# Kernel tuning notes

Hardware: AMD Instinct MI355X
Metric: run time of the kernel (lower is better)

Reference implementation:

```python
import jax, jax.numpy as jnp
import numpy as np

IM_SIZE = (256, 256)
OVERSAMP = 1.25
WIDTH = 6
BETA = float(np.pi * np.sqrt((WIDTH / OVERSAMP * (OVERSAMP - 0.5)) ** 2 - 0.8))
OS_SIZE = tuple(int(np.ceil(OVERSAMP * n)) for n in IM_SIZE)  # (320, 320)
D = 2


def _kb(x):
    # Kaiser-Bessel interpolation kernel: i0(beta*sqrt(1-x^2)) for |x|<=1 (sigpy convention)
    return jnp.i0(BETA * jnp.sqrt(jnp.maximum(1.0 - x * x, 0.0)))


def setup_inputs() -> dict:
    key = jax.random.key(0)
    k1, k2, k3 = jax.random.split(key, 3)
    N, C = 1, 8
    img_r = jax.random.normal(k1, (N, C) + IM_SIZE, dtype=jnp.float32)
    img_i = jax.random.normal(k2, (N, C) + IM_SIZE, dtype=jnp.float32)
    # trajectory in [-N_i/2, N_i/2] per the class docstring
    trj = (jax.random.uniform(k3, (N, 64, 4096, D), dtype=jnp.float32) - 0.5) * 256.0
    return {"img_r": img_r, "img_i": img_i, "trj": trj}


def _nufft_forward(img_r, img_i, trj):
    img = (img_r + 1j * img_i).astype(jnp.complex64)  # (N, C, H, W)
    nd = img.ndim
    # --- apodization (inverse FT of KB kernel), separable per axis ---
    for a in range(D):
        n, osn = IM_SIZE[a], OS_SIZE[a]
        idx = jnp.arange(n, dtype=jnp.float32)
        arg = jnp.sqrt(BETA ** 2 - (np.pi * WIDTH * (idx - n // 2) / osn) ** 2)
        apod = arg / jnp.sinh(arg)
        shape = [1] * nd
        shape[nd - D + a] = n
        img = img * apod.reshape(shape)
    # --- scale + centered zero-pad to oversampled grid ---
    img = img / np.sqrt(float(np.prod(IM_SIZE)))
    pads = [(0, 0)] * (nd - D) + [(((o - n) // 2), (o - n) - ((o - n) // 2))
                                  for n, o in zip(IM_SIZE, OS_SIZE)]
    img = jnp.pad(img, pads)
    # --- centered FFT (ifftshift -> fftn(norm=None) -> fftshift) ---
    axes = tuple(range(-D, 0))
    ksp_os = jnp.fft.fftshift(jnp.fft.fftn(jnp.fft.ifftshift(img, axes=axes), axes=axes), axes=axes)
    # --- scale trajectory to oversampled grid coordinates ---
    scale = jnp.array([OS_SIZE[a] / IM_SIZE[a] for a in range(D)], jnp.float32)
    shift = jnp.array([OS_SIZE[a] // 2 for a in range(D)], jnp.float32)
    coord = trj * scale + shift  # (N, R, S, 2)
    x0 = jnp.ceil(coord - WIDTH / 2.0)
    # --- KB interpolation: fixed 6x6 neighbor loop, vectorized gather over all points ---
    N = img.shape[0]
    out = jnp.zeros((N,) + img.shape[1:nd - D] + coord.shape[1:-1], jnp.complex64)

    def gather(grid, ix, iy):  # grid (C, Hos, Wos), ix/iy (R, S) -> (C, R, S)
        return grid[:, ix, iy]

    for dx in range(WIDTH):
        px = x0[..., 0] + dx
        wx = _kb((px - coord[..., 0]) / (WIDTH / 2.0))
        ix = px.astype(jnp.int32) % OS_SIZE[0]
        for dy in range(WIDTH):
            py = x0[..., 1] + dy
            wy = _kb((py - coord[..., 1]) / (WIDTH / 2.0))
            iy = py.astype(jnp.int32) % OS_SIZE[1]
            vals = jax.vmap(gather)(ksp_os, ix, iy)  # (N, C, R, S)
            out = out + vals * (wx * wy)[:, None, :, :]
    return out / (WIDTH ** D)


def reference(img_r, img_i, trj):
    return _nufft_forward(img_r, img_i, trj)
```

## Files before the change

kernel.cpp:

```cpp
#include <hip/hip_runtime.h>
#include <math.h>

#define NCH   8
#define IMN   256
#define OSN   320
#define NPTS  (64*4096)
#define KD    512
#define BETA_F   10.9551078f
#define BETA2_F  120.014389f
#define APOD_C   0.05890486225f
#define GROWS 326
#define GCOLS 328
#define GPITCH (GCOLS * NCH)

typedef unsigned short u16;
typedef unsigned int   u32;
typedef __attribute__((ext_vector_type(8))) short s16x8;
typedef __attribute__((ext_vector_type(4))) float f32x4;
typedef __attribute__((ext_vector_type(2))) float f32x2;

__device__ __forceinline__ u32 f2bf(float f) {
    u32 u = __float_as_uint(f);
    return (u + 0x7FFFu + ((u >> 16) & 1u)) >> 16;
}

__device__ __forceinline__ float i0f(float t) {
    if (t < 3.75f) {
        float y = t * t * (1.0f / 14.0625f);
        return 1.0f + y * (3.5156229f + y * (3.0899424f + y * (1.2067492f +
                     y * (0.2659732f + y * (0.0360768f + y * 0.0045813f)))));
    }
    float z = 3.75f / t;
    float p = 0.39894228f + z * (0.01328592f + z * (0.00225319f + z * (-0.00157565f +
              z * (0.00916281f + z * (-0.02057706f + z * (0.02635537f +
              z * (-0.01647633f + z * 0.00392377f)))))));
    return expf(t) * rsqrtf(t) * p;
}

__device__ __forceinline__ float apodf(int i) {
    float x = APOD_C * (float)(i - IMN / 2);
    float arg = sqrtf(BETA2_F - x * x);
    float e = expf(arg);
    float sh = 0.5f * (e - 1.0f / e);
    return arg / sh;
}

__global__ void prep(const float* __restrict__ r, const float* __restrict__ im,
                     u32* __restrict__ B1, u32* __restrict__ B2,
                     u32* __restrict__ A) {
    const int b = blockIdx.x, t = threadIdx.x;
    if (b < (OSN * IMN) / 256) {
        int idx = b * 256 + t;
        int k = idx >> 8, j = idx & 255;
        int p = (k * (j + 32)) % OSN;
        float th = (2.0f * (float)M_PI / (float)OSN) * (float)p;
        float s = ((k + j) & 1) ? -1.0f : 1.0f;
        float sn, cs;
        sincosf(th, &sn, &cs);
        float re = s * cs, imv = -s * sn;
        B1[idx] = f2bf(re) | (f2bf(-imv) << 16);
        B2[idx] = f2bf(imv) | (f2bf(re) << 16);
    } else {
        int idx = (b - (OSN * IMN) / 256) * 256 + t;
        int i2 = idx & 255, i1 = (idx >> 8) & 255;
        float w = apodf(i1) * apodf(i2) * (1.0f / 256.0f);
        A[idx] = f2bf(r[idx] * w) | (f2bf(im[idx] * w) << 16);
    }
}

__launch_bounds__(64)
__global__ void gemm1(const short* __restrict__ Abf, const short* __restrict__ B1,
                      const short* __restrict__ B2, short* __restrict__ Tb) {
    const int c = blockIdx.z;
    const int mBase = blockIdx.y * 32;
    const int nBase = blockIdx.x * 32;
    __shared__ short As[2][32][36], B1s[2][32][36], B2s[2][32][36];
    const int t = threadIdx.x;
    const int row = t >> 1, seg = (t & 1) * 16;
    const int fm = t & 15, fq = (t >> 4) * 8;
    const short* ap  = Abf + (long)(c * IMN + mBase + row) * KD + seg;
    const short* b1p = B1 + (long)(nBase + row) * KD + seg;
    const short* b2p = B2 + (long)(nBase + row) * KD + seg;
    f32x4 zz = {0.f, 0.f, 0.f, 0.f};
    f32x4 accRe[2][2], accIm[2][2];
    #pragma unroll
    for (int i = 0; i < 2; i++)
        #pragma unroll
        for (int j = 0; j < 2; j++) { accRe[i][j] = zz; accIm[i][j] = zz; }

    s16x8 c0 = *(const s16x8*)(ap);
    s16x8 c1 = *(const s16x8*)(ap + 8);
    s16x8 c2 = *(const s16x8*)(b1p);
    s16x8 c3 = *(const s16x8*)(b1p + 8);
    s16x8 c4 = *(const s16x8*)(b2p);
    s16x8 c5 = *(const s16x8*)(b2p + 8);

    #pragma unroll
    for (int kc = 0; kc < 16; kc++) {
        const int buf = kc & 1;
        *(s16x8*)&As [buf][row][seg]     = c0;
        *(s16x8*)&As [buf][row][seg + 8] = c1;
        *(s16x8*)&B1s[buf][row][seg]     = c2;
        *(s16x8*)&B1s[buf][row][seg + 8] = c3;
        *(s16x8*)&B2s[buf][row][seg]     = c4;
        *(s16x8*)&B2s[buf][row][seg + 8] = c5;
        if (kc < 15) {
            const int kb = (kc + 1) * 32;
            c0 = *(const s16x8*)(ap + kb);
            c1 = *(const s16x8*)(ap + kb + 8);
            c2 = *(const s16x8*)(b1p + kb);
            c3 = *(const s16x8*)(b1p + kb + 8);
            c4 = *(const s16x8*)(b2p + kb);
            c5 = *(const s16x8*)(b2p + kb + 8);
        }
        s16x8 a0  = *(const s16x8*)&As [buf][fm][fq];
        s16x8 a1  = *(const s16x8*)&As [buf][16 + fm][fq];
        s16x8 b10 = *(const s16x8*)&B1s[buf][fm][fq];
        s16x8 b11 = *(const s16x8*)&B1s[buf][16 + fm][fq];
        s16x8 b20 = *(const s16x8*)&B2s[buf][fm][fq];
        s16x8 b21 = *(const s16x8*)&B2s[buf][16 + fm][fq];
        accRe[0][0] = __builtin_amdgcn_mfma_f32_16x16x32_bf16(a0, b10, accRe[0][0], 0, 0, 0);
        accRe[0][1] = __builtin_amdgcn_mfma_f32_16x16x32_bf16(a0, b11, accRe[0][1], 0, 0, 0);
        accRe[1][0] = __builtin_amdgcn_mfma_f32_16x16x32_bf16(a1, b10, accRe[1][0], 0, 0, 0);
        accRe[1][1] = __builtin_amdgcn_mfma_f32_16x16x32_bf16(a1, b11, accRe[1][1], 0, 0, 0);
        accIm[0][0] = __builtin_amdgcn_mfma_f32_16x16x32_bf16(a0, b20, accIm[0][0], 0, 0, 0);
        accIm[0][1] = __builtin_amdgcn_mfma_f32_16x16x32_bf16(a0, b21, accIm[0][1], 0, 0, 0);
        accIm[1][0] = __builtin_amdgcn_mfma_f32_16x16x32_bf16(a1, b20, accIm[1][0], 0, 0, 0);
        accIm[1][1] = __builtin_amdgcn_mfma_f32_16x16x32_bf16(a1, b21, accIm[1][1], 0, 0, 0);
    }
    #pragma unroll
    for (int i = 0; i < 2; i++)
        #pragma unroll
        for (int j = 0; j < 2; j++) {
            int i1b = mBase + i * 16 + (t >> 4) * 4;
            int k2  = nBase + j * 16 + fm;
            s16x8 v;
            #pragma unroll
            for (int r = 0; r < 4; r++) {
                v[2 * r]     = (short)f2bf(accRe[i][j][r]);
                v[2 * r + 1] = (short)f2bf(accIm[i][j][r]);
            }
            *(s16x8*)(Tb + ((long)(c * OSN + k2)) * KD + 2 * i1b) = v;
        }
}

__launch_bounds__(64)
__global__ void gemm2(const short* __restrict__ B1, const short* __restrict__ B2,
                      const short* __restrict__ Tb, u32* __restrict__ Gb) {
    const int c = blockIdx.z;
    const int mBase = blockIdx.y * 32;
    const int nBase = blockIdx.x * 32;
    __shared__ short A1s[2][32][36], A2s[2][32][36], Bs[2][32][36];
    const int t = threadIdx.x;
    const int row = t >> 1, seg = (t & 1) * 16;
    const int fm = t & 15, fq = (t >> 4) * 8;
    const short* a1p = B1 + (long)(mBase + row) * KD + seg;
    const short* a2p = B2 + (long)(mBase + row) * KD + seg;
    const short* bp  = Tb + ((long)(c * OSN + nBase + row)) * KD + seg;
    f32x4 zz = {0.f, 0.f, 0.f, 0.f};
    f32x4 accRe[2][2], accIm[2][2];
    #pragma unroll
    for (int i = 0; i < 2; i++)
        #pragma unroll
        for (int j = 0; j < 2; j++) { accRe[i][j] = zz; accIm[i][j] = zz; }

    s16x8 c0 = *(const s16x8*)(a1p);
    s16x8 c1 = *(const s16x8*)(a1p + 8);
    s16x8 c2 = *(const s16x8*)(a2p);
    s16x8 c3 = *(const s16x8*)(a2p + 8);
    s16x8 c4 = *(const s16x8*)(bp);
    s16x8 c5 = *(const s16x8*)(bp + 8);

    #pragma unroll
    for (int kc = 0; kc < 16; kc++) {
        const int buf = kc & 1;
        *(s16x8*)&A1s[buf][row][seg]     = c0;
        *(s16x8*)&A1s[buf][row][seg + 8] = c1;
        *(s16x8*)&A2s[buf][row][seg]     = c2;
        *(s16x8*)&A2s[buf][row][seg + 8] = c3;
        *(s16x8*)&Bs [buf][row][seg]     = c4;
        *(s16x8*)&Bs [buf][row][seg + 8] = c5;
        if (kc < 15) {
            const int kb = (kc + 1) * 32;
            c0 = *(const s16x8*)(a1p + kb);
            c1 = *(const s16x8*)(a1p + kb + 8);
            c2 = *(const s16x8*)(a2p + kb);
            c3 = *(const s16x8*)(a2p + kb + 8);
            c4 = *(const s16x8*)(bp + kb);
            c5 = *(const s16x8*)(bp + kb + 8);
        }
        s16x8 a10 = *(const s16x8*)&A1s[buf][fm][fq];
        s16x8 a11 = *(const s16x8*)&A1s[buf][16 + fm][fq];
        s16x8 a20 = *(const s16x8*)&A2s[buf][fm][fq];
        s16x8 a21 = *(const s16x8*)&A2s[buf][16 + fm][fq];
        s16x8 b0  = *(const s16x8*)&Bs [buf][fm][fq];
        s16x8 b1  = *(const s16x8*)&Bs [buf][16 + fm][fq];
        accRe[0][0] = __builtin_amdgcn_mfma_f32_16x16x32_bf16(a10, b0, accRe[0][0], 0, 0, 0);
        accRe[0][1] = __builtin_amdgcn_mfma_f32_16x16x32_bf16(a10, b1, accRe[0][1], 0, 0, 0);
        accRe[1][0] = __builtin_amdgcn_mfma_f32_16x16x32_bf16(a11, b0, accRe[1][0], 0, 0, 0);
        accRe[1][1] = __builtin_amdgcn_mfma_f32_16x16x32_bf16(a11, b1, accRe[1][1], 0, 0, 0);
        accIm[0][0] = __builtin_amdgcn_mfma_f32_16x16x32_bf16(a20, b0, accIm[0][0], 0, 0, 0);
        accIm[0][1] = __builtin_amdgcn_mfma_f32_16x16x32_bf16(a20, b1, accIm[0][1], 0, 0, 0);
        accIm[1][0] = __builtin_amdgcn_mfma_f32_16x16x32_bf16(a21, b0, accIm[1][0], 0, 0, 0);
        accIm[1][1] = __builtin_amdgcn_mfma_f32_16x16x32_bf16(a21, b1, accIm[1][1], 0, 0, 0);
    }
    #pragma unroll
    for (int i = 0; i < 2; i++)
        #pragma unroll
        for (int j = 0; j < 2; j++) {
            int k2 = nBase + j * 16 + fm;
            int pc  = k2 + 3;
            int pc2 = (k2 < 3) ? (k2 + 323) : ((k2 >= 317) ? (k2 - 317) : -1);
            #pragma unroll
            for (int r = 0; r < 4; r++) {
                int k1 = mBase + i * 16 + (t >> 4) * 4 + r;
                u32 val = f2bf(accRe[i][j][r]) | (f2bf(accIm[i][j][r]) << 16);
                int pr  = k1 + 3;
                int pr2 = (k1 < 3) ? (k1 + 323) : ((k1 >= 317) ? (k1 - 317) : -1);
                Gb[(long)pr * GPITCH + pc * NCH + c] = val;
                if (pr2 >= 0)              Gb[(long)pr2 * GPITCH + pc  * NCH + c] = val;
                if (pc2 >= 0)              Gb[(long)pr  * GPITCH + pc2 * NCH + c] = val;
                if (pr2 >= 0 && pc2 >= 0)  Gb[(long)pr2 * GPITCH + pc2 * NCH + c] = val;
            }
        }
}

__global__ void interp_kernel(const float* __restrict__ trj,
                              const u32* __restrict__ grid,
                              u32* __restrict__ out) {
    const int t = threadIdx.x;
    __shared__ float wxs[128][6], wys[128][6];
    __shared__ int   x0s[128], y0s[128];

    {
        int ptl = t & 127, axis = t >> 7;
        int pt = blockIdx.x * 128 + ptl;
        float tv = trj[pt * 2 + axis];
        float cc = __fadd_rn(__fmul_rn(tv, 1.25f), 160.0f);
        float v0 = ceilf(__fadd_rn(cc, -3.0f));
        if (axis) y0s[ptl] = (int)v0; else x0s[ptl] = (int)v0;
        float* ws = axis ? wys[ptl] : wxs[ptl];
        #pragma unroll
        for (int d = 0; d < 6; d++) {
            float u = __fdiv_rn(__fsub_rn(v0 + (float)d, cc), 3.0f);
            ws[d] = i0f(BETA_F * sqrtf(fmaxf(1.0f - u * u, 0.0f)));
        }
    }
    __syncthreads();

    const int pl = t >> 1;
    const int h = t & 1;
    float wx[6], wy[6];
    #pragma unroll
    for (int d = 0; d < 6; d++) { wx[d] = wxs[pl][d]; wy[d] = wys[pl][d]; }
    const int px = x0s[pl] + 3;
    const int py = y0s[pl] + 3;
    const u32* g0 = grid + (long)px * GPITCH + py * NCH + h * 4;

    uint4 buf[2][6];
    #pragma unroll
    for (int dy = 0; dy < 6; dy++) buf[0][dy] = *(const uint4*)(g0 + dy * NCH);

    f32x2 a0 = {0.f, 0.f}, a1 = {0.f, 0.f}, a2 = {0.f, 0.f}, a3 = {0.f, 0.f};
    #pragma unroll
    for (int dx = 0; dx < 6; dx++) {
        if (dx < 5) {
            const u32* gn = g0 + (dx + 1) * GPITCH;
            #pragma unroll
            for (int dy = 0; dy < 6; dy++)
                buf[(dx + 1) & 1][dy] = *(const uint4*)(gn + dy * NCH);
        }
        float wxv = wx[dx];
        #pragma unroll
        for (int dy = 0; dy < 6; dy++) {
            uint4 g = buf[dx & 1][dy];
            float ww = wxv * wy[dy];
            f32x2 w2 = {ww, ww};
            f32x2 v0v = { __uint_as_float(g.x << 16), __uint_as_float(g.x & 0xFFFF0000u) };
            f32x2 v1v = { __uint_as_float(g.y << 16), __uint_as_float(g.y & 0xFFFF0000u) };
            f32x2 v2v = { __uint_as_float(g.z << 16), __uint_as_float(g.z & 0xFFFF0000u) };
            f32x2 v3v = { __uint_as_float(g.w << 16), __uint_as_float(g.w & 0xFFFF0000u) };
            a0 += v0v * w2;
            a1 += v1v * w2;
            a2 += v2v * w2;
            a3 += v3v * w2;
        }
    }
    f32x2 sc = {1.0f / 36.0f, 1.0f / 36.0f};
    a0 *= sc; a1 *= sc; a2 *= sc; a3 *= sc;

    __shared__ f32x2 lds[128][9];
    lds[pl][h * 4]     = a0;
    lds[pl][h * 4 + 1] = a1;
    lds[pl][h * 4 + 2] = a2;
    lds[pl][h * 4 + 3] = a3;
    __syncthreads();
    int c2 = t >> 5, p2 = t & 31;
    long ob = (long)c2 * NPTS + blockIdx.x * 128;
    #pragma unroll
    for (int k = 0; k < 4; k++) {
        f32x2 v = lds[p2 + 32 * k][c2];
        out[ob + p2 + 32 * k] = f2bf(v.y) | (f2bf(v.x) << 16);
    }
}

extern "C" void kernel_launch(void* const* d_in, const int* in_sizes, int n_in,
                              void* d_out, int out_size, void* d_ws, size_t ws_size,
                              hipStream_t stream) {
    const float* img_r = (const float*)d_in[0];
    const float* img_i = (const float*)d_in[1];
    const float* trj   = (const float*)d_in[2];

    char* ob = (char*)d_out;
    short* Tb  = (short*)(ob);
    u32*  B1u  = (u32*)(ob + 2621440);
    u32*  B2u  = (u32*)(ob + 2949120);
    u32*  Au   = (u32*)(ob + 3276800);
    u32*  Gb   = (u32*)d_ws;

    prep<<<(OSN * IMN) / 256 + (NCH * IMN * IMN) / 256, 256, 0, stream>>>(
        img_r, img_i, B1u, B2u, Au);
    gemm1<<<dim3(OSN / 32, IMN / 32, NCH), 64, 0, stream>>>(
        (const short*)Au, (const short*)B1u, (const short*)B2u, Tb);
    gemm2<<<dim3(OSN / 32, OSN / 32, NCH), 64, 0, stream>>>(
        (const short*)B1u, (const short*)B2u, Tb, Gb);
    interp_kernel<<<NPTS / 128, 256, 0, stream>>>(trj, Gb, (u32*)d_out);
}
```

Before: 115.9 us.

## Split interp work into 4 threads per point with all 36 gathers issued upfront

The interpolation kernel now gives each point four threads, each handling two channels with 8-byte loads, instead of two threads with 16-byte loads per point. Blocks cover 64 points, so twice as many blocks launch. All 36 neighbour loads are issued before any math rather than double-buffered row by row, and launch bounds are added to steer register use. The aim is more memory-level parallelism and thread-level parallelism for the scattered gathers, at the cost of narrower loads, more duplicated weight and address work per point, and higher register pressure from the 36-element buffer.

Measured after the change: 111.7 us. 3.6% less time.

```diff
diff --git a/kernel.cpp b/kernel.cpp
--- a/kernel.cpp
+++ b/kernel.cpp
@@ -225,16 +225,17 @@
         }
 }
 
+__launch_bounds__(256, 4)
 __global__ void interp_kernel(const float* __restrict__ trj,
                               const u32* __restrict__ grid,
                               u32* __restrict__ out) {
     const int t = threadIdx.x;
-    __shared__ float wxs[128][6], wys[128][6];
-    __shared__ int   x0s[128], y0s[128];
-
-    {
-        int ptl = t & 127, axis = t >> 7;
-        int pt = blockIdx.x * 128 + ptl;
+    __shared__ float wxs[64][6], wys[64][6];
+    __shared__ int   x0s[64], y0s[64];
+
+    if (t < 128) {
+        int ptl = t & 63, axis = t >> 6;
+        int pt = blockIdx.x * 64 + ptl;
         float tv = trj[pt * 2 + axis];
         float cc = __fadd_rn(__fmul_rn(tv, 1.25f), 160.0f);
         float v0 = ceilf(__fadd_rn(cc, -3.0f));
@@ -248,60 +249,50 @@
     }
     __syncthreads();
 
-    const int pl = t >> 1;
-    const int h = t & 1;
-    float wx[6], wy[6];
-    #pragma unroll
-    for (int d = 0; d < 6; d++) { wx[d] = wxs[pl][d]; wy[d] = wys[pl][d]; }
+    const int pl = t >> 2;
+    const int cp = (t & 3) * 2;
     const int px = x0s[pl] + 3;
     const int py = y0s[pl] + 3;
-    const u32* g0 = grid + (long)px * GPITCH + py * NCH + h * 4;
-
-    uint4 buf[2][6];
-    #pragma unroll
-    for (int dy = 0; dy < 6; dy++) buf[0][dy] = *(const uint4*)(g0 + dy * NCH);
-
-    f32x2 a0 = {0.f, 0.f}, a1 = {0.f, 0.f}, a2 = {0.f, 0.f}, a3 = {0.f, 0.f};
+    const u32* g0 = grid + (long)px * GPITCH + py * NCH + cp;
+
+    uint2 g[36];
+    #pragma unroll
+    for (int dx = 0; dx < 6; dx++)
+        #pragma unroll
+        for (int dy = 0; dy < 6; dy++)
+            g[dx * 6 + dy] = *(const uint2*)(g0 + dx * GPITCH + dy * NCH);
+
+    float wx[6], wy[6];
+    #pragma unroll
+    for (int d = 0; d < 6; d++) { wx[d] = wxs[pl][d]; wy[d] = wys[pl][d]; }
+
+    float re0 = 0.f, im0 = 0.f, re1 = 0.f, im1 = 0.f;
     #pragma unroll
     for (int dx = 0; dx < 6; dx++) {
-        if (dx < 5) {
-            const u32* gn = g0 + (dx + 1) * GPITCH;
-            #pragma unroll
-            for (int dy = 0; dy < 6; dy++)
-                buf[(dx + 1) & 1][dy] = *(const uint4*)(gn + dy * NCH);
-        }
         float wxv = wx[dx];
         #pragma unroll
         for (int dy = 0; dy < 6; dy++) {
-            uint4 g = buf[dx & 1][dy];
+            uint2 gv = g[dx * 6 + dy];
             float ww = wxv * wy[dy];
-            f32x2 w2 = {ww, ww};
-            f32x2 v0v = { __uint_as_float(g.x << 16), __uint_as_float(g.x & 0xFFFF0000u) };
-            f32x2 v1v = { __uint_as_float(g.y << 16), __uint_as_float(g.y & 0xFFFF0000u) };
-            f32x2 v2v = { __uint_as_float(g.z << 16), __uint_as_float(g.z & 0xFFFF0000u) };
-            f32x2 v3v = { __uint_as_float(g.w << 16), __uint_as_float(g.w & 0xFFFF0000u) };
-            a0 += v0v * w2;
-            a1 += v1v * w2;
-            a2 += v2v * w2;
-            a3 += v3v * w2;
-        }
-    }
-    f32x2 sc = {1.0f / 36.0f, 1.0f / 36.0f};
-    a0 *= sc; a1 *= sc; a2 *= sc; a3 *= sc;
-
-    __shared__ f32x2 lds[128][9];
-    lds[pl][h * 4]     = a0;
-    lds[pl][h * 4 + 1] = a1;
-    lds[pl][h * 4 + 2] = a2;
-    lds[pl][h * 4 + 3] = a3;
+            re0 += __uint_as_float(gv.x << 16) * ww;
+            im0 += __uint_as_float(gv.x & 0xFFFF0000u) * ww;
+            re1 += __uint_as_float(gv.y << 16) * ww;
+            im1 += __uint_as_float(gv.y & 0xFFFF0000u) * ww;
+        }
+    }
+    re0 *= (1.0f / 36.0f); im0 *= (1.0f / 36.0f);
+    re1 *= (1.0f / 36.0f); im1 *= (1.0f / 36.0f);
+
+    __shared__ float2 lds[64][9];
+    lds[pl][cp]     = make_float2(re0, im0);
+    lds[pl][cp + 1] = make_float2(re1, im1);
     __syncthreads();
     int c2 = t >> 5, p2 = t & 31;
-    long ob = (long)c2 * NPTS + blockIdx.x * 128;
-    #pragma unroll
-    for (int k = 0; k < 4; k++) {
-        f32x2 v = lds[p2 + 32 * k][c2];
-        out[ob + p2 + 32 * k] = f2bf(v.y) | (f2bf(v.x) << 16);
-    }
+    float2 va = lds[p2][c2];
+    float2 vb = lds[p2 + 32][c2];
+    long ob = (long)c2 * NPTS + blockIdx.x * 64;
+    out[ob + p2]      = f2bf(va.y) | (f2bf(va.x) << 16);
+    out[ob + p2 + 32] = f2bf(vb.y) | (f2bf(vb.x) << 16);
 }
 
 extern "C" void kernel_launch(void* const* d_in, const int* in_sizes, int n_in,
@@ -324,5 +315,5 @@
         (const short*)Au, (const short*)B1u, (const short*)B2u, Tb);
     gemm2<<<dim3(OSN / 32, OSN / 32, NCH), 64, 0, stream>>>(
         (const short*)B1u, (const short*)B2u, Tb, Gb);
-    interp_kernel<<<NPTS / 128, 256, 0, stream>>>(trj, Gb, (u32*)d_out);
-}
+    interp_kernel<<<NPTS / 64, 256, 0, stream>>>(trj, Gb, (u32*)d_out);
+}
```
